# Kernel tuning notes

Hardware: AMD Instinct MI355X
Metric: run time of the kernel (lower is better)

## Reference

```python
import jax, jax.numpy as jnp
import numpy as np

SLOPE = 25.0  # snntorch fast_sigmoid default surrogate slope

@jax.custom_vjp
def spike(u):
    return (u > 0).astype(u.dtype)

def _spike_fwd(u):
    return spike(u), u

def _spike_bwd(u, g):
    return (g / (1.0 + SLOPE * jnp.abs(u)) ** 2,)

spike.defvjp(_spike_fwd, _spike_bwd)

def fake_quant(W):
    # brevitas-style int8 per-tensor symmetric fake-quant with STE
    s = jnp.max(jnp.abs(W)) / 127.0
    q = jnp.clip(jnp.round(W / s), -127.0, 127.0) * s
    return W + jax.lax.stop_gradient(q - W)

def setup_inputs() -> dict:
    key = jax.random.key(0)
    ks = jax.random.split(key, 8)
    B, NIN, T = 256, 512, 256
    H1, H2, OUT = 512, 512, 128
    data = jax.random.normal(ks[0], (B, NIN, T), dtype=jnp.float32)
    W1 = jax.random.normal(ks[1], (H1, NIN), dtype=jnp.float32) / np.sqrt(NIN)
    W2 = jax.random.normal(ks[2], (H2, H1), dtype=jnp.float32) / np.sqrt(H1)
    Wrec = jax.random.normal(ks[3], (H2, H2), dtype=jnp.float32) / np.sqrt(H2)
    W3 = jax.random.normal(ks[4], (OUT, H2), dtype=jnp.float32) / np.sqrt(H2)
    beta = jnp.float32(0.9)
    th = jnp.float32(1.0)
    return {"data": data, "W1": W1, "W2": W2, "Wrec": Wrec, "W3": W3,
            "beta1": beta, "th1": th, "beta_r": beta, "th_r": th,
            "beta2": beta, "th2": th}

def reference(data, W1, W2, Wrec, W3, beta1, th1, beta_r, th_r, beta2, th2):
    B = data.shape[0]
    H1, H2, OUT = W1.shape[0], W2.shape[0], W3.shape[0]
    W1q = fake_quant(W1)
    W2q = fake_quant(W2)
    Wrq = fake_quant(Wrec)
    W3q = fake_quant(W3)
    b1 = jnp.clip(beta1, 0.0, 1.0)
    br = jnp.clip(beta_r, 0.0, 1.0)
    b2 = jnp.clip(beta2, 0.0, 1.0)
    # time-major input: [T, B, NIN]
    xs = jnp.transpose(data, (2, 0, 1))

    def step(carry, x):
        m1, mr, sr, m2 = carry
        # leaky1: reset zero, reset_delay=False
        m1 = b1 * m1 + x @ W1q.T
        s1 = spike(m1 - th1)
        m1 = m1 * (1.0 - s1)
        # recurrent LIF (RLeaky-like), reset zero, reset_delay=True:
        # previous spike resets the membrane at the start of this step
        h = s1 @ W2q.T + sr @ Wrq.T
        mr = (br * mr + h) * (1.0 - sr)
        sr = spike(mr - th_r)
        # leaky2: reset zero, reset_delay=False
        m2 = b2 * m2 + sr @ W3q.T
        s2 = spike(m2 - th2)
        m2 = m2 * (1.0 - s2)
        return (m1, mr, sr, m2), s2

    init = (jnp.zeros((B, H1), jnp.float32),
            jnp.zeros((B, H2), jnp.float32),
            jnp.zeros((B, H2), jnp.float32),
            jnp.zeros((B, OUT), jnp.float32))
    _, spk_rec = jax.lax.scan(step, init, xs)
    return spk_rec  # [T, B, OUT]
```

## Files before the change

kernel.cpp:

```cpp
#include <hip/hip_runtime.h>

#define B_   256
#define NIN_ 512
#define T_   256
#define H1_  512
#define H2_  512
#define OUT_ 128

typedef __attribute__((ext_vector_type(4))) int i32x4;
typedef __attribute__((address_space(1))) const unsigned int* gl_cu;
typedef __attribute__((address_space(3))) unsigned int* ls_u;

__global__ void absmax_k(const float* __restrict__ W1, const float* __restrict__ W2,
                         const float* __restrict__ Wr, const float* __restrict__ W3,
                         float* __restrict__ scales) {
  const float* W; int n;
  switch (blockIdx.x) {
    case 0:  W = W1; n = H1_ * NIN_; break;
    case 1:  W = W2; n = H2_ * H1_;  break;
    case 2:  W = Wr; n = H2_ * H2_;  break;
    default: W = W3; n = OUT_ * H2_; break;
  }
  int tid = threadIdx.x;
  float m = 0.f;
  const float4* W4 = (const float4*)W;
  int n4 = n >> 2;
  for (int i = tid; i < n4; i += 256) {
    float4 v = W4[i];
    m = fmaxf(m, fmaxf(fmaxf(fabsf(v.x), fabsf(v.y)), fmaxf(fabsf(v.z), fabsf(v.w))));
  }
  __shared__ float red[256];
  red[tid] = m;
  __syncthreads();
  for (int s = 128; s > 0; s >>= 1) {
    if (tid < s) red[tid] = fmaxf(red[tid], red[tid + s]);
    __syncthreads();
  }
  if (tid == 0) scales[blockIdx.x] = red[0] / 127.0f;
}

__global__ void quant_all_k(const float* __restrict__ W1, const float* __restrict__ W2,
                            const float* __restrict__ Wr, const float* __restrict__ W3,
                            const float* __restrict__ scales,
                            float* __restrict__ W1qT, signed char* __restrict__ W2i8,
                            signed char* __restrict__ WrT, signed char* __restrict__ W3i8) {
  const int blk = blockIdx.x;
  if (blk < 1024) {
    int idx = blk * 256 + threadIdx.x;
    int h = idx & (H1_ - 1), i = idx >> 9;
    float s = scales[0];
    float q = rintf(W1[h * NIN_ + i] / s);
    q = fminf(fmaxf(q, -127.f), 127.f);
    W1qT[idx] = q * s;
  } else if (blk < 2048) {
    int idx = (blk - 1024) * 256 + threadIdx.x;
    float s = scales[1];
    float q = rintf(W2[idx] / s);
    q = fminf(fmaxf(q, -127.f), 127.f);
    W2i8[idx] = (signed char)q;
  } else if (blk < 3072) {
    int idx = (blk - 2048) * 256 + threadIdx.x;
    int r = idx >> 9, c = idx & (H2_ - 1);
    float s = scales[2];
    float q = rintf(Wr[idx] / s);
    q = fminf(fmaxf(q, -127.f), 127.f);
    WrT[(size_t)c * H2_ + r] = (signed char)q;
  } else {
    int idx = (blk - 3072) * 256 + threadIdx.x;
    float s = scales[3];
    float q = rintf(W3[idx] / s);
    q = fminf(fmaxf(q, -127.f), 127.f);
    W3i8[idx] = (signed char)q;
  }
}

__global__ __launch_bounds__(512, 6) void gemm_cur1_k(const float* __restrict__ data,
                                                      const float* __restrict__ W1qT,
                                                      float* __restrict__ cur1) {
  const int b  = blockIdx.y;
  const int t0 = (blockIdx.x >> 2) << 7;
  const int h0 = (blockIdx.x & 3) << 7;
  const int tid = threadIdx.x;

  __shared__ float As[2][16][128];
  __shared__ float Bs[2][16][128];

  const int ty = tid >> 4, tx = tid & 15;
  const int wv = tid >> 6;
  const int ln = tid & 63;

  float acc[4][8];
#pragma unroll
  for (int i = 0; i < 4; i++)
#pragma unroll
    for (int j = 0; j < 8; j++) acc[i][j] = 0.f;

  const float* dbase = data + (size_t)b * NIN_ * T_;

  auto issue = [&](int kb, int buf) {
    const int kr = (wv << 1) + (ln >> 5);
    const float* ga = dbase + (size_t)(kb + kr) * T_ + t0 + ((ln & 31) << 2);
    __builtin_amdgcn_global_load_lds((gl_cu)ga, (ls_u)&As[buf][wv << 1][0], 16, 0, 0);
    const float* gb = W1qT + (size_t)(kb + kr) * H1_ + h0 + ((ln & 31) << 2);
    __builtin_amdgcn_global_load_lds((gl_cu)gb, (ls_u)&Bs[buf][wv << 1][0], 16, 0, 0);
  };

  issue(0, 0);

  for (int p = 0; p < 32; p++) {
    const int cur = p & 1;
    __syncthreads();
    if (p < 31) issue((p + 1) << 4, cur ^ 1);
#pragma unroll
    for (int k = 0; k < 16; k++) {
      float4 A0 = *(const float4*)&As[cur][k][ty * 4];
      float4 B0 = *(const float4*)&Bs[cur][k][tx * 4];
      float4 B1 = *(const float4*)&Bs[cur][k][64 + tx * 4];
      float a[4] = {A0.x, A0.y, A0.z, A0.w};
      float w[8] = {B0.x, B0.y, B0.z, B0.w, B1.x, B1.y, B1.z, B1.w};
#pragma unroll
      for (int i = 0; i < 4; i++)
#pragma unroll
        for (int j = 0; j < 8; j++)
          acc[i][j] = fmaf(a[i], w[j], acc[i][j]);
    }
  }

#pragma unroll
  for (int i = 0; i < 4; i++) {
    int row = ty * 4 + i;
    float* op = cur1 + (size_t)(t0 + row) * (B_ * H1_) + (size_t)b * H1_ + h0;
    float4 cA = {acc[i][0], acc[i][1], acc[i][2], acc[i][3]};
    float4 cB = {acc[i][4], acc[i][5], acc[i][6], acc[i][7]};
    *(float4*)(op + tx * 4)      = cA;
    *(float4*)(op + 64 + tx * 4) = cB;
  }
}

__global__ __launch_bounds__(256) void scan1_k(const float* __restrict__ cur1,
                                               unsigned char* __restrict__ s1u,
                                               const float* __restrict__ beta1p,
                                               const float* __restrict__ th1p) {
  const int n = blockIdx.x * 256 + threadIdx.x;
  const float b1 = fminf(fmaxf(beta1p[0], 0.f), 1.f);
  const float th1 = th1p[0];
  const size_t S = (size_t)B_ * H1_;
  float m1 = 0.f;
  for (int t = 0; t < T_; t += 4) {
    float c0 = cur1[(size_t)t * S + n];
    float c1 = cur1[(size_t)(t + 1) * S + n];
    float c2 = cur1[(size_t)(t + 2) * S + n];
    float c3 = cur1[(size_t)(t + 3) * S + n];
    m1 = b1 * m1 + c0; bool s0 = m1 - th1 > 0.f; if (s0) m1 = 0.f;
    s1u[(size_t)t * S + n] = s0;
    m1 = b1 * m1 + c1; bool s1 = m1 - th1 > 0.f; if (s1) m1 = 0.f;
    s1u[(size_t)(t + 1) * S + n] = s1;
    m1 = b1 * m1 + c2; bool s2 = m1 - th1 > 0.f; if (s2) m1 = 0.f;
    s1u[(size_t)(t + 2) * S + n] = s2;
    m1 = b1 * m1 + c3; bool s3 = m1 - th1 > 0.f; if (s3) m1 = 0.f;
    s1u[(size_t)(t + 3) * S + n] = s3;
  }
}

__global__ __launch_bounds__(256) void gemm_spk_k(const unsigned char* __restrict__ A8,
                                                  const signed char* __restrict__ Bw,
                                                  float* __restrict__ C, int N) {
  __shared__ __align__(16) signed char As[2][128 * 80];
  __shared__ __align__(16) signed char Bs[2][128 * 80];
  const int tid = threadIdx.x;
  const int m0 = blockIdx.y << 7;
  const int n0 = blockIdx.x << 7;
  const int lane = tid & 63, wave = tid >> 6;
  const int quad = lane >> 4, lm = lane & 15;
  const int wm = wave << 5;

  i32x4 acc[2][8];
#pragma unroll
  for (int s = 0; s < 2; s++)
#pragma unroll
    for (int n = 0; n < 8; n++) acc[s][n] = (i32x4){0, 0, 0, 0};

  const int row = tid >> 2;
  const int offB = (tid & 3) << 4;

  uint4 av[2], bv[2];
  auto gload = [&](int kb) {
#pragma unroll
    for (int i = 0; i < 2; i++) {
      const int r = row + (i << 6);
      av[i] = *(const uint4*)(A8 + (size_t)(m0 + r) * 512 + kb + offB);
      bv[i] = *(const uint4*)(Bw + (size_t)(n0 + r) * 512 + kb + offB);
    }
  };

  gload(0);
  int buf = 0;
  for (int kb8 = 0; kb8 < 8; kb8++) {
#pragma unroll
    for (int i = 0; i < 2; i++) {
      const int r = row + (i << 6);
      *(uint4*)&As[buf][r * 80 + offB] = av[i];
      *(uint4*)&Bs[buf][r * 80 + offB] = bv[i];
    }
    __syncthreads();
    if (kb8 < 7) gload((kb8 + 1) << 6);
    i32x4 a0 = *(const i32x4*)&As[buf][(wm + lm) * 80 + (quad << 4)];
    i32x4 a1 = *(const i32x4*)&As[buf][(wm + 16 + lm) * 80 + (quad << 4)];
    i32x4 bq[8];
#pragma unroll
    for (int n = 0; n < 8; n++)
      bq[n] = *(const i32x4*)&Bs[buf][((n << 4) + lm) * 80 + (quad << 4)];
#pragma unroll
    for (int n = 0; n < 8; n++) {
      acc[0][n] = __builtin_amdgcn_mfma_i32_16x16x64_i8(a0, bq[n], acc[0][n], 0, 0, 0);
      acc[1][n] = __builtin_amdgcn_mfma_i32_16x16x64_i8(a1, bq[n], acc[1][n], 0, 0, 0);
    }
    buf ^= 1;
  }

#pragma unroll
  for (int s = 0; s < 2; s++)
#pragma unroll
    for (int n = 0; n < 8; n++) {
      int orow = m0 + wm + (s << 4) + quad * 4;
      int col = n0 + (n << 4) + lm;
#pragma unroll
      for (int r = 0; r < 4; r++)
        C[(size_t)(orow + r) * N + col] = (float)acc[s][n][r];
    }
}

__device__ __forceinline__ void unp_add(unsigned w, int* a) {
  int iw = (int)w;
  a[0] += (iw << 24) >> 24;
  a[1] += (iw << 16) >> 24;
  a[2] += (iw << 8) >> 24;
  a[3] += iw >> 24;
}

__global__ __launch_bounds__(1024) void recurrent_k(
    const float* __restrict__ cur2a,
    const signed char* __restrict__ WrT,
    unsigned char* __restrict__ sru,
    const float* __restrict__ scales,
    const float* __restrict__ betarp, const float* __restrict__ thrp) {
  const int b = blockIdx.x;
  const int tid = threadIdx.x;
  const float s2sc = scales[1];
  const float srsc = scales[2];
  const float br = fminf(fmaxf(betarp[0], 0.f), 1.f);
  const float thr = thrp[0];

  const unsigned* WrT4 = (const unsigned*)WrT;

  __shared__ unsigned WrL[256 * 128];
  __shared__ int red[8][H2_];
  __shared__ int lstLo[2][256];
  __shared__ int lstHi[2][256];
  __shared__ int ncLo[2], ncHi[2];

  {
    const uint4* src = (const uint4*)WrT4;
    uint4* dst = (uint4*)WrL;
    for (int i = tid; i < 8192; i += 1024) dst[i] = src[i];
  }
  if (tid < 2) { ncLo[tid] = 0; ncHi[tid] = 0; }
  __syncthreads();

  float mr = 0.f, sr_own = 0.f;
  const int g = tid >> 7;
  const int c = tid & 127;

  for (int t = 0; t < T_; t++) {
    const int old = t & 1, nxt = old ^ 1;
    float c2 = 0.f;
    if (tid < H2_) c2 = cur2a[((size_t)t * B_ + b) * H2_ + tid];
    if (tid == 1022) ncLo[nxt] = 0;
    if (tid == 1023) ncHi[nxt] = 0;
    const int nLo = ncLo[old];
    const int nHi = ncHi[old];
    const int* LLo = lstLo[old];
    const int* LHi = lstHi[old];

    int a4[4] = {0, 0, 0, 0};
    {
      int k = g;
      for (; k + 56 < nLo; k += 64) {
        int i0 = LLo[k],      i1 = LLo[k + 8],  i2 = LLo[k + 16], i3 = LLo[k + 24];
        int i4 = LLo[k + 32], i5 = LLo[k + 40], i6 = LLo[k + 48], i7 = LLo[k + 56];
        unsigned w0 = WrL[(i0 << 7) + c], w1 = WrL[(i1 << 7) + c];
        unsigned w2 = WrL[(i2 << 7) + c], w3 = WrL[(i3 << 7) + c];
        unsigned w4 = WrL[(i4 << 7) + c], w5 = WrL[(i5 << 7) + c];
        unsigned w6 = WrL[(i6 << 7) + c], w7 = WrL[(i7 << 7) + c];
        unp_add(w0, a4); unp_add(w1, a4); unp_add(w2, a4); unp_add(w3, a4);
        unp_add(w4, a4); unp_add(w5, a4); unp_add(w6, a4); unp_add(w7, a4);
      }
      for (; k + 24 < nLo; k += 32) {
        int i0 = LLo[k], i1 = LLo[k + 8], i2 = LLo[k + 16], i3 = LLo[k + 24];
        unsigned w0 = WrL[(i0 << 7) + c], w1 = WrL[(i1 << 7) + c];
        unsigned w2 = WrL[(i2 << 7) + c], w3 = WrL[(i3 << 7) + c];
        unp_add(w0, a4); unp_add(w1, a4); unp_add(w2, a4); unp_add(w3, a4);
      }
      for (; k < nLo; k += 8) unp_add(WrL[(LLo[k] << 7) + c], a4);
    }
    {
      int k = g;
      for (; k + 56 < nHi; k += 64) {
        int i0 = LHi[k],      i1 = LHi[k + 8],  i2 = LHi[k + 16], i3 = LHi[k + 24];
        int i4 = LHi[k + 32], i5 = LHi[k + 40], i6 = LHi[k + 48], i7 = LHi[k + 56];
        unsigned w0 = WrT4[(i0 << 7) + c], w1 = WrT4[(i1 << 7) + c];
        unsigned w2 = WrT4[(i2 << 7) + c], w3 = WrT4[(i3 << 7) + c];
        unsigned w4 = WrT4[(i4 << 7) + c], w5 = WrT4[(i5 << 7) + c];
        unsigned w6 = WrT4[(i6 << 7) + c], w7 = WrT4[(i7 << 7) + c];
        unp_add(w0, a4); unp_add(w1, a4); unp_add(w2, a4); unp_add(w3, a4);
        unp_add(w4, a4); unp_add(w5, a4); unp_add(w6, a4); unp_add(w7, a4);
      }
      for (; k + 24 < nHi; k += 32) {
        int i0 = LHi[k], i1 = LHi[k + 8], i2 = LHi[k + 16], i3 = LHi[k + 24];
        unsigned w0 = WrT4[(i0 << 7) + c], w1 = WrT4[(i1 << 7) + c];
        unsigned w2 = WrT4[(i2 << 7) + c], w3 = WrT4[(i3 << 7) + c];
        unp_add(w0, a4); unp_add(w1, a4); unp_add(w2, a4); unp_add(w3, a4);
      }
      for (; k < nHi; k += 8) unp_add(WrT4[(LHi[k] << 7) + c], a4);
    }
    *(int4*)&red[g][c << 2] = make_int4(a4[0], a4[1], a4[2], a4[3]);
    __syncthreads();

    bool spike = false;
    if (tid < H2_) {
      int acc = red[0][tid] + red[1][tid] + red[2][tid] + red[3][tid]
              + red[4][tid] + red[5][tid] + red[6][tid] + red[7][tid];
      float h = s2sc * c2 + srsc * (float)acc;
      mr = (br * mr + h) * (1.f - sr_own);
      sr_own = (mr - thr > 0.f) ? 1.f : 0.f;
      sru[((size_t)t * B_ + b) * H2_ + tid] = (unsigned char)(sr_own != 0.f);
      spike = (sr_own != 0.f);
    }
    unsigned long long bm = __ballot(spike);
    if (bm != 0ull) {
      const int lane = tid & 63;
      const int ldr = (int)__ffsll((long long)bm) - 1;
      int* cnt = (tid < 256) ? &ncLo[nxt] : &ncHi[nxt];
      int* dst = (tid < 256) ? lstLo[nxt] : lstHi[nxt];
      int base = 0;
      if (lane == ldr) base = atomicAdd(cnt, (int)__popcll(bm));
      base = __shfl(base, ldr);
      if (spike)
        dst[base + (int)__popcll(bm & ((1ull << lane) - 1ull))] = tid;
    }
    __syncthreads();
  }
}

__global__ __launch_bounds__(256) void scan3_k(const float* __restrict__ cur3,
                                               float* __restrict__ out,
                                               const float* __restrict__ scales,
                                               const float* __restrict__ beta2p,
                                               const float* __restrict__ th2p) {
  const int n = blockIdx.x * 256 + threadIdx.x;
  const float s3sc = scales[3];
  const float b2 = fminf(fmaxf(beta2p[0], 0.f), 1.f);
  const float th2 = th2p[0];
  const size_t S = (size_t)B_ * OUT_;
  float m2 = 0.f;
  for (int t = 0; t < T_; t += 4) {
    float v0 = cur3[(size_t)t * S + n];
    float v1 = cur3[(size_t)(t + 1) * S + n];
    float v2 = cur3[(size_t)(t + 2) * S + n];
    float v3 = cur3[(size_t)(t + 3) * S + n];
    m2 = b2 * m2 + s3sc * v0; float p0 = (m2 - th2 > 0.f) ? 1.f : 0.f; m2 *= (1.f - p0);
    out[(size_t)t * S + n] = p0;
    m2 = b2 * m2 + s3sc * v1; float p1 = (m2 - th2 > 0.f) ? 1.f : 0.f; m2 *= (1.f - p1);
    out[(size_t)(t + 1) * S + n] = p1;
    m2 = b2 * m2 + s3sc * v2; float p2 = (m2 - th2 > 0.f) ? 1.f : 0.f; m2 *= (1.f - p2);
    out[(size_t)(t + 2) * S + n] = p2;
    m2 = b2 * m2 + s3sc * v3; float p3 = (m2 - th2 > 0.f) ? 1.f : 0.f; m2 *= (1.f - p3);
    out[(size_t)(t + 3) * S + n] = p3;
  }
}

extern "C" void kernel_launch(void* const* d_in, const int* in_sizes, int n_in,
                              void* d_out, int out_size, void* d_ws, size_t ws_size,
                              hipStream_t stream) {
  const float* data  = (const float*)d_in[0];
  const float* W1    = (const float*)d_in[1];
  const float* W2    = (const float*)d_in[2];
  const float* Wr    = (const float*)d_in[3];
  const float* W3    = (const float*)d_in[4];
  const float* beta1 = (const float*)d_in[5];
  const float* th1   = (const float*)d_in[6];
  const float* betar = (const float*)d_in[7];
  const float* thr   = (const float*)d_in[8];
  const float* beta2 = (const float*)d_in[9];
  const float* th2   = (const float*)d_in[10];

  char* ws = (char*)d_ws;
  float*         scales = (float*)ws;
  float*         W1qT   = (float*)(ws + 4096);
  signed char*   W2i8   = (signed char*)(ws + 4096 + 1048576);
  signed char*   W3i8   = (signed char*)(ws + 4096 + 1048576 + 524288);
  signed char*   WrT    = (signed char*)(ws + 4096 + 1048576 + 524288 + 131072);
  float*         regA   = (float*)(ws + (size_t)4194304);
  unsigned char* regB   = (unsigned char*)(ws + (size_t)4194304 + 134217728);

  float* cur1  = regA;
  float* cur2a = regA;
  float* cur3  = regA;
  unsigned char* s1u = regB;
  unsigned char* sru = regB + (size_t)33554432;

  hipLaunchKernelGGL(absmax_k, dim3(4), dim3(256), 0, stream, W1, W2, Wr, W3, scales);
  hipLaunchKernelGGL(quant_all_k, dim3(3328), dim3(256), 0, stream,
                     W1, W2, Wr, W3, scales, W1qT, W2i8, WrT, W3i8);

  hipLaunchKernelGGL(gemm_cur1_k, dim3(8, 256), dim3(512), 0, stream, data, W1qT, cur1);
  hipLaunchKernelGGL(scan1_k, dim3((B_ * H1_) / 256), dim3(256), 0, stream, cur1, s1u, beta1, th1);
  hipLaunchKernelGGL(gemm_spk_k, dim3(4, 512), dim3(256), 0, stream, s1u, W2i8, cur2a, H2_);
  hipLaunchKernelGGL(recurrent_k, dim3(256), dim3(1024), 0, stream, cur2a, WrT, sru, scales, betar, thr);
  hipLaunchKernelGGL(gemm_spk_k, dim3(1, 512), dim3(256), 0, stream, sru, W3i8, cur3, OUT_);
  hipLaunchKernelGGL(scan3_k, dim3((B_ * OUT_) / 256), dim3(256), 0, stream, cur3, (float*)d_out, scales, beta2, th2);
}
```

Baseline: 1.035 ms.

## Parallelize weight absmax across blocks, swap GEMM grid order, deepen scan unrolling

The per-tensor absmax now runs on 64 blocks per weight tensor instead of one, combining partial maxima with an atomicMax on the float bit pattern. Scales are then derived inside the quant kernel. The spike GEMM grid is transposed so consecutive blocks walk along M and share the same weight column tile, which may improve L2 reuse of B. The scan kernels load 8 timesteps ahead instead of 4 to hide more memory latency. The cost is an extra memset and atomics, plus slightly more registers in the scans.

```diff
diff --git a/kernel.cpp b/kernel.cpp
--- a/kernel.cpp
+++ b/kernel.cpp
@@ -11,21 +11,25 @@
 typedef __attribute__((address_space(1))) const unsigned int* gl_cu;
 typedef __attribute__((address_space(3))) unsigned int* ls_u;
 
-__global__ void absmax_k(const float* __restrict__ W1, const float* __restrict__ W2,
-                         const float* __restrict__ Wr, const float* __restrict__ W3,
-                         float* __restrict__ scales) {
-  const float* W; int n;
-  switch (blockIdx.x) {
-    case 0:  W = W1; n = H1_ * NIN_; break;
-    case 1:  W = W2; n = H2_ * H1_;  break;
-    case 2:  W = Wr; n = H2_ * H2_;  break;
-    default: W = W3; n = OUT_ * H2_; break;
-  }
+__global__ __launch_bounds__(256) void absmax_k(const float* __restrict__ W1,
+                                                const float* __restrict__ W2,
+                                                const float* __restrict__ Wr,
+                                                const float* __restrict__ W3,
+                                                unsigned* __restrict__ smax) {
+  const int tens = blockIdx.x >> 6;
+  const int sub  = blockIdx.x & 63;
+  const float* W; int n4;
+  switch (tens) {
+    case 0:  W = W1; n4 = (H1_ * NIN_) >> 2; break;
+    case 1:  W = W2; n4 = (H2_ * H1_) >> 2;  break;
+    case 2:  W = Wr; n4 = (H2_ * H2_) >> 2;  break;
+    default: W = W3; n4 = (OUT_ * H2_) >> 2; break;
+  }
+  const int per = n4 >> 6;
+  const float4* W4 = (const float4*)W + sub * per;
   int tid = threadIdx.x;
   float m = 0.f;
-  const float4* W4 = (const float4*)W;
-  int n4 = n >> 2;
-  for (int i = tid; i < n4; i += 256) {
+  for (int i = tid; i < per; i += 256) {
     float4 v = W4[i];
     m = fmaxf(m, fmaxf(fmaxf(fabsf(v.x), fabsf(v.y)), fmaxf(fabsf(v.z), fabsf(v.w))));
   }
@@ -36,38 +40,41 @@
     if (tid < s) red[tid] = fmaxf(red[tid], red[tid + s]);
     __syncthreads();
   }
-  if (tid == 0) scales[blockIdx.x] = red[0] / 127.0f;
+  if (tid == 0) atomicMax(smax + tens, __float_as_uint(red[0]));
 }
 
 __global__ void quant_all_k(const float* __restrict__ W1, const float* __restrict__ W2,
                             const float* __restrict__ Wr, const float* __restrict__ W3,
-                            const float* __restrict__ scales,
+                            const unsigned* __restrict__ smax,
+                            float* __restrict__ scales,
                             float* __restrict__ W1qT, signed char* __restrict__ W2i8,
                             signed char* __restrict__ WrT, signed char* __restrict__ W3i8) {
   const int blk = blockIdx.x;
+  if (blk == 0 && threadIdx.x < 4)
+    scales[threadIdx.x] = __uint_as_float(smax[threadIdx.x]) / 127.0f;
   if (blk < 1024) {
     int idx = blk * 256 + threadIdx.x;
     int h = idx & (H1_ - 1), i = idx >> 9;
-    float s = scales[0];
+    float s = __uint_as_float(smax[0]) / 127.0f;
     float q = rintf(W1[h * NIN_ + i] / s);
     q = fminf(fmaxf(q, -127.f), 127.f);
     W1qT[idx] = q * s;
   } else if (blk < 2048) {
     int idx = (blk - 1024) * 256 + threadIdx.x;
-    float s = scales[1];
+    float s = __uint_as_float(smax[1]) / 127.0f;
     float q = rintf(W2[idx] / s);
     q = fminf(fmaxf(q, -127.f), 127.f);
     W2i8[idx] = (signed char)q;
   } else if (blk < 3072) {
     int idx = (blk - 2048) * 256 + threadIdx.x;
     int r = idx >> 9, c = idx & (H2_ - 1);
-    float s = scales[2];
+    float s = __uint_as_float(smax[2]) / 127.0f;
     float q = rintf(Wr[idx] / s);
     q = fminf(fmaxf(q, -127.f), 127.f);
     WrT[(size_t)c * H2_ + r] = (signed char)q;
   } else {
     int idx = (blk - 3072) * 256 + threadIdx.x;
-    float s = scales[3];
+    float s = __uint_as_float(smax[3]) / 127.0f;
     float q = rintf(W3[idx] / s);
     q = fminf(fmaxf(q, -127.f), 127.f);
     W3i8[idx] = (signed char)q;
@@ -146,19 +153,17 @@
   const float th1 = th1p[0];
   const size_t S = (size_t)B_ * H1_;
   float m1 = 0.f;
-  for (int t = 0; t < T_; t += 4) {
-    float c0 = cur1[(size_t)t * S + n];
-    float c1 = cur1[(size_t)(t + 1) * S + n];
-    float c2 = cur1[(size_t)(t + 2) * S + n];
-    float c3 = cur1[(size_t)(t + 3) * S + n];
-    m1 = b1 * m1 + c0; bool s0 = m1 - th1 > 0.f; if (s0) m1 = 0.f;
-    s1u[(size_t)t * S + n] = s0;
-    m1 = b1 * m1 + c1; bool s1 = m1 - th1 > 0.f; if (s1) m1 = 0.f;
-    s1u[(size_t)(t + 1) * S + n] = s1;
-    m1 = b1 * m1 + c2; bool s2 = m1 - th1 > 0.f; if (s2) m1 = 0.f;
-    s1u[(size_t)(t + 2) * S + n] = s2;
-    m1 = b1 * m1 + c3; bool s3 = m1 - th1 > 0.f; if (s3) m1 = 0.f;
-    s1u[(size_t)(t + 3) * S + n] = s3;
+  for (int t = 0; t < T_; t += 8) {
+    float c[8];
+#pragma unroll
+    for (int j = 0; j < 8; j++) c[j] = cur1[(size_t)(t + j) * S + n];
+#pragma unroll
+    for (int j = 0; j < 8; j++) {
+      m1 = b1 * m1 + c[j];
+      bool s = m1 - th1 > 0.f;
+      if (s) m1 = 0.f;
+      s1u[(size_t)(t + j) * S + n] = s;
+    }
   }
 }
 
@@ -168,8 +173,8 @@
   __shared__ __align__(16) signed char As[2][128 * 80];
   __shared__ __align__(16) signed char Bs[2][128 * 80];
   const int tid = threadIdx.x;
-  const int m0 = blockIdx.y << 7;
-  const int n0 = blockIdx.x << 7;
+  const int m0 = blockIdx.x << 7;
+  const int n0 = blockIdx.y << 7;
   const int lane = tid & 63, wave = tid >> 6;
   const int quad = lane >> 4, lm = lane & 15;
   const int wm = wave << 5;
@@ -363,19 +368,17 @@
   const float th2 = th2p[0];
   const size_t S = (size_t)B_ * OUT_;
   float m2 = 0.f;
-  for (int t = 0; t < T_; t += 4) {
-    float v0 = cur3[(size_t)t * S + n];
-    float v1 = cur3[(size_t)(t + 1) * S + n];
-    float v2 = cur3[(size_t)(t + 2) * S + n];
-    float v3 = cur3[(size_t)(t + 3) * S + n];
-    m2 = b2 * m2 + s3sc * v0; float p0 = (m2 - th2 > 0.f) ? 1.f : 0.f; m2 *= (1.f - p0);
-    out[(size_t)t * S + n] = p0;
-    m2 = b2 * m2 + s3sc * v1; float p1 = (m2 - th2 > 0.f) ? 1.f : 0.f; m2 *= (1.f - p1);
-    out[(size_t)(t + 1) * S + n] = p1;
-    m2 = b2 * m2 + s3sc * v2; float p2 = (m2 - th2 > 0.f) ? 1.f : 0.f; m2 *= (1.f - p2);
-    out[(size_t)(t + 2) * S + n] = p2;
-    m2 = b2 * m2 + s3sc * v3; float p3 = (m2 - th2 > 0.f) ? 1.f : 0.f; m2 *= (1.f - p3);
-    out[(size_t)(t + 3) * S + n] = p3;
+  for (int t = 0; t < T_; t += 8) {
+    float v[8];
+#pragma unroll
+    for (int j = 0; j < 8; j++) v[j] = cur3[(size_t)(t + j) * S + n];
+#pragma unroll
+    for (int j = 0; j < 8; j++) {
+      m2 = b2 * m2 + s3sc * v[j];
+      float p = (m2 - th2 > 0.f) ? 1.f : 0.f;
+      m2 *= (1.f - p);
+      out[(size_t)(t + j) * S + n] = p;
+    }
   }
 }
 
@@ -396,6 +399,7 @@
 
   char* ws = (char*)d_ws;
   float*         scales = (float*)ws;
+  unsigned*      smax   = (unsigned*)(ws + 64);
   float*         W1qT   = (float*)(ws + 4096);
   signed char*   W2i8   = (signed char*)(ws + 4096 + 1048576);
   signed char*   W3i8   = (signed char*)(ws + 4096 + 1048576 + 524288);
@@ -409,14 +413,15 @@
   unsigned char* s1u = regB;
   unsigned char* sru = regB + (size_t)33554432;
 
-  hipLaunchKernelGGL(absmax_k, dim3(4), dim3(256), 0, stream, W1, W2, Wr, W3, scales);
+  hipMemsetAsync(smax, 0, 16, stream);
+  hipLaunchKernelGGL(absmax_k, dim3(256), dim3(256), 0, stream, W1, W2, Wr, W3, smax);
   hipLaunchKernelGGL(quant_all_k, dim3(3328), dim3(256), 0, stream,
-                     W1, W2, Wr, W3, scales, W1qT, W2i8, WrT, W3i8);
+                     W1, W2, Wr, W3, smax, scales, W1qT, W2i8, WrT, W3i8);
 
   hipLaunchKernelGGL(gemm_cur1_k, dim3(8, 256), dim3(512), 0, stream, data, W1qT, cur1);
   hipLaunchKernelGGL(scan1_k, dim3((B_ * H1_) / 256), dim3(256), 0, stream, cur1, s1u, beta1, th1);
-  hipLaunchKernelGGL(gemm_spk_k, dim3(4, 512), dim3(256), 0, stream, s1u, W2i8, cur2a, H2_);
+  hipLaunchKernelGGL(gemm_spk_k, dim3(512, 4), dim3(256), 0, stream, s1u, W2i8, cur2a, H2_);
   hipLaunchKernelGGL(recurrent_k, dim3(256), dim3(1024), 0, stream, cur2a, WrT, sru, scales, betar, thr);
-  hipLaunchKernelGGL(gemm_spk_k, dim3(1, 512), dim3(256), 0, stream, sru, W3i8, cur3, OUT_);
+  hipLaunchKernelGGL(gemm_spk_k, dim3(512, 1), dim3(256), 0, stream, sru, W3i8, cur3, OUT_);
   hipLaunchKernelGGL(scan3_k, dim3((B_ * OUT_) / 256), dim3(256), 0, stream, cur3, (float*)d_out, scales, beta2, th2);
 }
```

New measurement: 986.2 us (median of 2 runs). -4.7%, faster.
